# Kernel optimization log

Hardware: AMD Instinct MI355X
Metric: run time of the kernel (lower is better)

The kernel has to match this reference:

```python
import jax, jax.numpy as jnp
import numpy as np

TARGET = 560   # target_size
EPS = 1e-8


def setup_inputs() -> dict:
    key = jax.random.key(0)
    k1, k2, k3, k4 = jax.random.split(key, 4)
    B, K, D, C, N = 2, 1600, 1024, 256, 32
    feats = jax.random.normal(k1, (B, K, D), dtype=jnp.float32)
    embedding = jax.random.normal(k2, (C, D), dtype=jnp.float32)
    # valid boxes: x_min,y_min in [0, 400), side in [16, 160) => min_box_size satisfied, in-bounds
    xy_min = jax.random.randint(k3, (B, N, 2), 0, TARGET - 160)
    wh = jax.random.randint(k4, (B, N, 2), 16, 160)
    xy_max = jnp.minimum(xy_min + wh, TARGET)
    boxes = jnp.concatenate([xy_min, xy_max], axis=-1).astype(jnp.int32)  # (B,N,4) = x_min,y_min,x_max,y_max
    return {"feats": feats, "embedding": embedding, "boxes": boxes}


def reference(feats, embedding, boxes):
    # feats: (B,K,D) patch features, embedding: (C,D) class prototypes, boxes: (B,N,4) int
    B, K, D = feats.shape
    C = embedding.shape[0]
    P = int(np.sqrt(K))  # patch_2d_size

    # --- get_cosim_mini_batch (normalize=True), fused as a single GEMM + norm ---
    dot = jnp.einsum('bkd,cd->bck', feats, embedding)          # (B,C,K)
    feats_norm = jnp.linalg.norm(feats, axis=-1)               # (B,K)
    emb_norm = jnp.linalg.norm(embedding, axis=-1)             # (C,)
    cosim = dot / (feats_norm[:, None, :] * emb_norm[None, :, None] + EPS)
    cosim = cosim.reshape(B, C, P, P)
    cosim = jax.image.resize(cosim, (B, C, TARGET, TARGET), method='bicubic')  # (B,C,560,560)
    # single scale -> stack().mean(0) is identity

    # --- box mean pooling: cosim[b,:,y_min:y_max-1, x_min:x_max-1].mean((1,2)) via masks ---
    x_min, y_min, x_max, y_max = boxes[..., 0], boxes[..., 1], boxes[..., 2], boxes[..., 3]
    r = jnp.arange(TARGET)
    my = ((r[None, None, :] >= y_min[..., None]) & (r[None, None, :] <= y_max[..., None] - 2)).astype(cosim.dtype)  # (B,N,H)
    mx = ((r[None, None, :] >= x_min[..., None]) & (r[None, None, :] <= x_max[..., None] - 2)).astype(cosim.dtype)  # (B,N,W)
    counts = my.sum(-1) * mx.sum(-1)                           # (B,N)
    pooled = jnp.einsum('bnh,bnw,bchw->bnc', my, mx, cosim)    # (B,N,C)
    box_sim = pooled / counts[..., None]
    return box_sim.reshape(-1, C)
```

## Files before the change

### kernel.cpp

```cpp
#include <hip/hip_runtime.h>
#include <hip/hip_bf16.h>
#include <math.h>

#define TGT 560
#define B_ 2
#define K_ 1600
#define D_ 1024
#define C_ 256
#define N_ 32
#define P_ 40
#define KC_ 32
#define KCHUNK 50

#define OFF_IFN ((size_t)0)
#define OFF_IEN (OFF_IFN + (size_t)B_ * K_)
#define OFF_BOXW (OFF_IEN + (size_t)C_)
#define OFF_G   ((size_t)16384)

__global__ __launch_bounds__(256) void kA(const float* __restrict__ feats,
                                          const float* __restrict__ emb,
                                          const int* __restrict__ boxes,
                                          float* __restrict__ ws) {
    __shared__ float shm[80];
    const int r = blockIdx.x;
    const int t = threadIdx.x;
    if (r < B_ * K_ + C_) {
        const float* src;
        float* dst;
        if (r < B_ * K_) { src = feats + (size_t)r * D_; dst = ws + OFF_IFN + r; }
        else             { src = emb + (size_t)(r - B_ * K_) * D_; dst = ws + OFF_IEN + (r - B_ * K_); }
        float4 v = ((const float4*)src)[t];
        float s = v.x * v.x + v.y * v.y + v.z * v.z + v.w * v.w;
        #pragma unroll
        for (int off = 32; off > 0; off >>= 1) s += __shfl_down(s, off, 64);
        if ((t & 63) == 0) shm[t >> 6] = s;
        __syncthreads();
        if (t == 0) {
            float tot = shm[0] + shm[1] + shm[2] + shm[3];
            *dst = 1.0f / sqrtf(tot);
        }
    } else {
        const int bn = r - (B_ * K_ + C_);
        ((float4*)(ws + OFF_G + (size_t)bn * D_))[t] = make_float4(0.f, 0.f, 0.f, 0.f);
        if (t < 80) shm[t] = 0.f;
        __syncthreads();
        const int* bx = boxes + bn * 4;
        const int xmin = bx[0], ymin = bx[1], xmax = bx[2], ymax = bx[3];
        const float invcnt = 1.0f / ((float)(ymax - 1 - ymin) * (float)(xmax - 1 - xmin));
        const int axis = t >> 7;
        const int rr = t & 127;
        const int lo = (axis ? xmin : ymin);
        const int hi = (axis ? xmax : ymax) - 2;
        for (int h = lo + rr; h <= hi; h += 128) {
            float sf = ((float)h + 0.5f) * (1.0f / 14.0f) - 0.5f;
            int jf = (int)floorf(sf);
            float w[4];
            float norm = 0.f;
            #pragma unroll
            for (int dj = -1; dj <= 2; ++dj) {
                int j = jf + dj;
                float x = fabsf(sf - (float)j);
                float wv = ((1.5f * x - 2.5f) * x) * x + 1.f;
                if (x >= 1.f) wv = ((-0.5f * x + 2.5f) * x - 4.f) * x + 2.f;
                if (x >= 2.f) wv = 0.f;
                if (j < 0 || j >= P_) wv = 0.f;
                w[dj + 1] = wv;
                norm += wv;
            }
            float inv = 1.0f / norm;
            #pragma unroll
            for (int dj = 0; dj < 4; ++dj) {
                int j = jf - 1 + dj;
                if (w[dj] != 0.f) atomicAdd(&shm[axis * P_ + j], w[dj] * inv);
            }
        }
        __syncthreads();
        if (t < 80) {
            float val = shm[t];
            if (t < P_) val *= invcnt;
            ws[OFF_BOXW + (size_t)bn * 80 + t] = val;
        }
    }
}

__global__ __launch_bounds__(256) void kB(const float* __restrict__ feats,
                                          const float* __restrict__ ws,
                                          float* __restrict__ g) {
    __shared__ float sw[N_ * 80];
    __shared__ float vlds[KCHUNK * N_];
    const int bid = blockIdx.x;
    const int b = bid >> 7;
    const int rest = bid & 127;
    const int kc = rest >> 2;
    const int dt = rest & 3;
    const int t = threadIdx.x;
    const int k0 = kc * KCHUNK;

    for (int i = t; i < N_ * 80; i += 256)
        sw[i] = ws[OFF_BOXW + (size_t)b * N_ * 80 + i];
    __syncthreads();
    const float* ifn = ws + OFF_IFN + (size_t)b * K_;
    for (int i = t; i < KCHUNK * N_; i += 256) {
        int kk = i >> 5, n = i & 31;
        int k = k0 + kk;
        int pq = k / P_;
        int q = k - pq * P_;
        vlds[kk * N_ + n] = sw[n * 80 + pq] * sw[n * 80 + P_ + q] * ifn[k];
    }
    __syncthreads();

    float acc[N_];
    #pragma unroll
    for (int n = 0; n < N_; ++n) acc[n] = 0.f;

    const float* fp = feats + ((size_t)b * K_ + k0) * D_ + dt * 256 + t;
    #pragma unroll
    for (int gi = 0; gi < 5; ++gi) {
        float f[10];
        #pragma unroll
        for (int u = 0; u < 10; ++u) f[u] = fp[(size_t)(gi * 10 + u) * D_];
        #pragma unroll
        for (int u = 0; u < 10; ++u) {
            const float4* vp = (const float4*)&vlds[(gi * 10 + u) * N_];
            #pragma unroll
            for (int j = 0; j < 8; ++j) {
                float4 v4 = vp[j];
                acc[4 * j + 0] = fmaf(v4.x, f[u], acc[4 * j + 0]);
                acc[4 * j + 1] = fmaf(v4.y, f[u], acc[4 * j + 1]);
                acc[4 * j + 2] = fmaf(v4.z, f[u], acc[4 * j + 2]);
                acc[4 * j + 3] = fmaf(v4.w, f[u], acc[4 * j + 3]);
            }
        }
    }
    float* o = g + (size_t)b * N_ * D_ + dt * 256 + t;
    #pragma unroll
    for (int n = 0; n < N_; ++n) atomicAdd(&o[(size_t)n * D_], acc[n]);
}

__global__ __launch_bounds__(256) void kC(const float* __restrict__ emb,
                                          const float* __restrict__ g,
                                          const float* __restrict__ ien,
                                          float* __restrict__ out) {
    __shared__ float4 g4[D_ / 4];
    __shared__ float part[256];
    const int bid = blockIdx.x;
    const int bn = bid >> 2;
    const int ct = bid & 3;
    const int t = threadIdx.x;

    g4[t] = ((const float4*)(g + (size_t)bn * D_))[t];
    __syncthreads();

    const int cl = t & 63;
    const int dq = t >> 6;
    const int c = ct * 64 + cl;
    const float4* e4 = (const float4*)(emb + (size_t)c * D_) + dq * 64;
    const float4* gg = g4 + dq * 64;
    float partial = 0.f;
    #pragma unroll 8
    for (int i = 0; i < 64; ++i) {
        float4 e = e4[i];
        float4 gv = gg[i];
        partial += e.x * gv.x + e.y * gv.y + e.z * gv.z + e.w * gv.w;
    }
    part[t] = partial;
    __syncthreads();
    if (t < 64) {
        int c2 = ct * 64 + t;
        float val = part[t] + part[64 + t] + part[128 + t] + part[192 + t];
        out[(size_t)bn * C_ + c2] = val * ien[c2];
    }
}

extern "C" void kernel_launch(void* const* d_in, const int* in_sizes, int n_in,
                              void* d_out, int out_size, void* d_ws, size_t ws_size,
                              hipStream_t stream) {
    const float* feats = (const float*)d_in[0];
    const float* emb   = (const float*)d_in[1];
    const int*   boxes = (const int*)d_in[2];
    float* out = (float*)d_out;
    float* ws  = (float*)d_ws;

    kA<<<B_ * K_ + C_ + B_ * N_, 256, 0, stream>>>(feats, emb, boxes, ws);
    kB<<<B_ * KC_ * 4, 256, 0, stream>>>(feats, ws, ws + OFF_G);
    kC<<<B_ * N_ * 4, 256, 0, stream>>>(emb, ws + OFF_G, ws + OFF_IEN, out);
}
```

Before: 94.86 us.

## Retile final projection kernel to reuse embedding rows across four boxes

The final GEMV-like kernel now has each block handle 4 box rows and 16 classes. Each wave loads contiguous embedding rows with coalesced float4 accesses and reduces them with wave shuffles. Each embedding load is reused across four box vectors, which cuts redundant global traffic on the embedding matrix. The cost is more registers and shuffle reductions, and the kernel is small so the effect on total time may be limited.

```diff
diff --git a/kernel.cpp b/kernel.cpp
--- a/kernel.cpp
+++ b/kernel.cpp
@@ -141,34 +141,54 @@
                                           const float* __restrict__ g,
                                           const float* __restrict__ ien,
                                           float* __restrict__ out) {
-    __shared__ float4 g4[D_ / 4];
-    __shared__ float part[256];
+    __shared__ float4 g4sh[4][D_ / 4];
+    __shared__ float part[16][4];
     const int bid = blockIdx.x;
-    const int bn = bid >> 2;
-    const int ct = bid & 3;
+    const int bng = bid >> 4;
+    const int ct  = bid & 15;
     const int t = threadIdx.x;
-
-    g4[t] = ((const float4*)(g + (size_t)bn * D_))[t];
-    __syncthreads();
-
-    const int cl = t & 63;
-    const int dq = t >> 6;
-    const int c = ct * 64 + cl;
-    const float4* e4 = (const float4*)(emb + (size_t)c * D_) + dq * 64;
-    const float4* gg = g4 + dq * 64;
-    float partial = 0.f;
-    #pragma unroll 8
-    for (int i = 0; i < 64; ++i) {
-        float4 e = e4[i];
-        float4 gv = gg[i];
-        partial += e.x * gv.x + e.y * gv.y + e.z * gv.z + e.w * gv.w;
-    }
-    part[t] = partial;
+    const int lane = t & 63;
+    const int wv = t >> 6;
+
+    #pragma unroll
+    for (int bn = 0; bn < 4; ++bn)
+        g4sh[bn][t] = ((const float4*)(g + (size_t)(bng * 4 + bn) * D_))[t];
+    __syncthreads();
+
+    float p[4][4];
+    #pragma unroll
+    for (int cc = 0; cc < 4; ++cc)
+        #pragma unroll
+        for (int bn = 0; bn < 4; ++bn) p[cc][bn] = 0.f;
+
+    #pragma unroll
+    for (int i = 0; i < 4; ++i) {
+        float4 gv[4];
+        #pragma unroll
+        for (int bn = 0; bn < 4; ++bn) gv[bn] = g4sh[bn][lane + 64 * i];
+        #pragma unroll
+        for (int cc = 0; cc < 4; ++cc) {
+            const int c = ct * 16 + wv * 4 + cc;
+            float4 e = ((const float4*)(emb + (size_t)c * D_))[lane + 64 * i];
+            #pragma unroll
+            for (int bn = 0; bn < 4; ++bn)
+                p[cc][bn] += e.x * gv[bn].x + e.y * gv[bn].y + e.z * gv[bn].z + e.w * gv[bn].w;
+        }
+    }
+    #pragma unroll
+    for (int cc = 0; cc < 4; ++cc) {
+        #pragma unroll
+        for (int bn = 0; bn < 4; ++bn) {
+            float v = p[cc][bn];
+            #pragma unroll
+            for (int off = 32; off > 0; off >>= 1) v += __shfl_down(v, off, 64);
+            if (lane == 0) part[wv * 4 + cc][bn] = v;
+        }
+    }
     __syncthreads();
     if (t < 64) {
-        int c2 = ct * 64 + t;
-        float val = part[t] + part[64 + t] + part[128 + t] + part[192 + t];
-        out[(size_t)bn * C_ + c2] = val * ien[c2];
+        const int c = t >> 2, bn = t & 3;
+        out[(size_t)(bng * 4 + bn) * C_ + ct * 16 + c] = part[c][bn] * ien[ct * 16 + c];
     }
 }
 
@@ -183,5 +203,5 @@
 
     kA<<<B_ * K_ + C_ + B_ * N_, 256, 0, stream>>>(feats, emb, boxes, ws);
     kB<<<B_ * KC_ * 4, 256, 0, stream>>>(feats, ws, ws + OFF_G);
-    kC<<<B_ * N_ * 4, 256, 0, stream>>>(emb, ws + OFF_G, ws + OFF_IEN, out);
-}
+    kC<<<256, 256, 0, stream>>>(emb, ws + OFF_G, ws + OFF_IEN, out);
+}
```

After: 90.92 us. 4.2% less time.
